# Optimization experiments

Hardware: AMD Instinct MI355X
Metric: run time of the kernel (lower is better)

## Reference

```python
import jax, jax.numpy as jnp
import numpy as np

N = 2048  # nodes; num_node_features == N per __init__
E = 65536 # directed edges (avg degree 32)
H1, H2 = 32, 20


def setup_inputs() -> dict:
    key = jax.random.key(0)
    ks = jax.random.split(key, 10)
    u = lambda k, shape, fan: jax.random.uniform(k, shape, jnp.float32, -1.0, 1.0) / np.sqrt(fan)
    x = jax.random.normal(ks[0], (N, N), jnp.float32)
    edge_index = jax.random.randint(ks[1], (2, E), 0, N, jnp.int64)
    return {
        'x': x,
        'edge_index': edge_index,
        'W1': u(ks[2], (N, H1), N),   'b1': u(ks[3], (H1,), N),
        'W2': u(ks[4], (H1, H2), H1), 'b2': u(ks[5], (H2,), H1),
        'aW': u(ks[6], (H2, N * N), H2), 'ab': u(ks[7], (N * N,), H2),
        'cW': u(ks[8], (H2, 1), H2),  'cb': u(ks[9], (1,), H2),
    }


def gcn_conv(x, edge_index, W, b):
    # GCNConv: D^{-1/2} (A + I) D^{-1/2} X W + b, aggregated at target nodes
    loop = jnp.arange(N)
    src = jnp.concatenate([edge_index[0], loop])
    dst = jnp.concatenate([edge_index[1], loop])
    deg = jax.ops.segment_sum(jnp.ones_like(dst, dtype=x.dtype), dst, num_segments=N)
    dinv = jnp.where(deg > 0, jax.lax.rsqrt(deg), 0.0)
    norm = dinv[src] * dinv[dst]                      # [E+N]
    h = x @ W                                         # [N, out]
    msg = h[src] * norm[:, None]                      # gather + scale
    return jax.ops.segment_sum(msg, dst, num_segments=N) + b


def reference(x, edge_index, W1, b1, W2, b2, aW, ab, cW, cb):
    h = jax.nn.relu(gcn_conv(x, edge_index, W1, b1))
    h = jax.nn.relu(gcn_conv(h, edge_index, W2, b2))
    critic_output = (h @ cW + cb).mean(axis=0)        # [1]
    x_actor = h.mean(axis=0)                          # [20]
    logits = (x_actor @ aW + ab).reshape(N, N)
    probs = jax.nn.softmax(logits, axis=1)
    flat = probs.reshape(-1)
    # Faithful replication of the sequential two-max scan: the second 'max'
    # is the running max just before the final update, i.e. the argmax of the
    # prefix strictly before the global argmax (0,0 if argmax is at flat[0]).
    idx1 = jnp.argmax(flat)
    masked = jnp.where(jnp.arange(N * N) < idx1, flat, -jnp.inf)
    idx2 = jnp.argmax(masked)  # argmax over all -inf -> 0, matching (si,sj)=(0,0)
    actions = jnp.stack([
        jnp.stack([idx1 // N, idx1 % N]),
        jnp.stack([idx2 // N, idx2 % N]),
    ])  # [2, 2] int
    # Faithful to original: indexes the FLATTENED probs with the (i,j) pairs
    log_probs = -jnp.log(flat[actions])               # [2, 2]
    return actions, log_probs, critic_output
```

## Files before the change

### kernel.cpp

```cpp
#include <hip/hip_runtime.h>
#include <hip/hip_bf16.h>
#include <math.h>

#define NN_NODES 2048
#define NE 65536
#define H1C 32
#define H2C 20
#define AW_STRIDE 4194304ull

__global__ void k_deg(const int* __restrict__ ei, int* __restrict__ deg) {
    int e = blockIdx.x * 256 + threadIdx.x;
    if (e < NE) atomicAdd(&deg[ei[NE + e]], 1);
}

__global__ void k_scan(const int* __restrict__ deg, float* __restrict__ dinv,
                       int* __restrict__ off) {
    __shared__ int s[1024];
    int t = threadIdx.x;
    int d0 = deg[2 * t], d1 = deg[2 * t + 1];
    dinv[2 * t]     = rsqrtf((float)(d0 + 1));
    dinv[2 * t + 1] = rsqrtf((float)(d1 + 1));
    s[t] = d0 + d1;
    __syncthreads();
    for (int o = 1; o < 1024; o <<= 1) {
        int add = (t >= o) ? s[t - o] : 0;
        __syncthreads();
        s[t] += add;
        __syncthreads();
    }
    int excl = (t > 0) ? s[t - 1] : 0;
    off[2 * t] = excl;
    off[2 * t + 1] = excl + d0;
    if (t == 1023) off[2048] = s[1023];
}

__global__ void k_scatter(const int* __restrict__ ei, const float* __restrict__ dinv,
                          const int* __restrict__ off, int* __restrict__ cnt,
                          int* __restrict__ csr_src, float* __restrict__ csr_norm) {
    int e = blockIdx.x * 256 + threadIdx.x;
    if (e >= NE) return;
    int s = ei[e], d = ei[NE + e];
    int pos = off[d] + atomicAdd(&cnt[d], 1);
    csr_src[pos] = s;
    csr_norm[pos] = dinv[s] * dinv[d];
}

__global__ __launch_bounds__(256) void k_gemm1(const float* __restrict__ X,
                                               const float* __restrict__ W1,
                                               float* __restrict__ h_tmp) {
    __shared__ float Xs[32][33];
    __shared__ __align__(16) float Ws[32][32];
    int t = threadIdx.x;
    int rg = blockIdx.x >> 3, kc = blockIdx.x & 7;
    int r0 = rg * 32;
    int r = t >> 3, c4 = (t & 7) * 4;
    float4 acc = {0.f, 0.f, 0.f, 0.f};
    for (int kt = 0; kt < 8; ++kt) {
        int k0 = kc * 256 + kt * 32;
#pragma unroll
        for (int i = 0; i < 4; ++i) {
            int id = t + i * 256;
            int rr = id >> 5, kk = id & 31;
            Xs[rr][kk] = X[(size_t)(r0 + rr) * 2048 + k0 + kk];
            Ws[rr][kk] = W1[(size_t)(k0 + rr) * 32 + kk];
        }
        __syncthreads();
#pragma unroll
        for (int kk = 0; kk < 32; ++kk) {
            float a = Xs[r][kk];
            float4 b = *(const float4*)&Ws[kk][c4];
            acc.x += a * b.x; acc.y += a * b.y; acc.z += a * b.z; acc.w += a * b.w;
        }
        __syncthreads();
    }
    float* dst = &h_tmp[(size_t)(r0 + r) * 32 + c4];
    atomicAdd(dst + 0, acc.x);
    atomicAdd(dst + 1, acc.y);
    atomicAdd(dst + 2, acc.z);
    atomicAdd(dst + 3, acc.w);
}

template <int C>
__global__ __launch_bounds__(256) void k_agg(const float* __restrict__ h,
                                             const float* __restrict__ csr_norm,
                                             const int* __restrict__ csr_src,
                                             const int* __restrict__ off,
                                             const float* __restrict__ dinv,
                                             const float* __restrict__ bias,
                                             float* __restrict__ out) {
    int n = blockIdx.x;
    int t = threadIdx.x;
    int c = t & 31, s = t >> 5;
    __shared__ float red[8][32];
    float acc = 0.f;
    int e0 = off[n], e1 = off[n + 1];
    if (c < C) {
        for (int e = e0 + s; e < e1; e += 8) {
            int src = csr_src[e];
            acc += h[(size_t)src * C + c] * csr_norm[e];
        }
    }
    red[s][c] = acc;
    __syncthreads();
    if (t < 32) {
        float v = red[0][t];
#pragma unroll
        for (int i = 1; i < 8; ++i) v += red[i][t];
        if (t < C) {
            float dn = dinv[n];
            v += h[(size_t)n * C + t] * dn * dn + bias[t];
            out[(size_t)n * C + t] = fmaxf(v, 0.f);
        }
    }
}

__global__ __launch_bounds__(256) void k_gemm2(const float* __restrict__ h1,
                                               const float* __restrict__ W2,
                                               float* __restrict__ h2t) {
    __shared__ float Ws[H1C * H2C];
    int t = threadIdx.x;
    for (int i = t; i < H1C * H2C; i += 256) Ws[i] = W2[i];
    __syncthreads();
    int id = blockIdx.x * 256 + t;
    int n = id / 20, c = id % 20;
    const float* hr = &h1[(size_t)n * 32];
    float acc = 0.f;
#pragma unroll
    for (int k = 0; k < 32; ++k) acc += hr[k] * Ws[k * 20 + c];
    h2t[(size_t)n * 20 + c] = acc;
}

__global__ __launch_bounds__(640) void k_xa(const float* __restrict__ h2,
                                            float* __restrict__ xa_sum) {
    __shared__ float red[640];
    int t = threadIdx.x;
    int nl = t / 20, c = t % 20;
    int n = blockIdx.x * 32 + nl;
    red[t] = h2[(size_t)n * 20 + c];
    __syncthreads();
    for (int o = 16; o >= 1; o >>= 1) {
        if (nl < o) red[t] += red[(nl + o) * 20 + c];
        __syncthreads();
    }
    if (t < 20) atomicAdd(&xa_sum[t], red[t]);
}

__global__ __launch_bounds__(256) void k_rows(const float* __restrict__ aW,
                                              const float* __restrict__ ab,
                                              const float* __restrict__ xa_sum,
                                              float* __restrict__ rowM,
                                              float* __restrict__ rowZ,
                                              int* __restrict__ rowC) {
    __shared__ float xa[20];
    __shared__ float redf[256];
    __shared__ int redi[256];
    int t = threadIdx.x;
    int row = blockIdx.x;
    if (t < 20) xa[t] = xa_sum[t] * (1.0f / 2048.0f);
    __syncthreads();
    size_t base = (size_t)row * 2048;
    float l[8];
#pragma unroll
    for (int u = 0; u < 2; ++u) {
        int j0 = u * 1024 + t * 4;
        float4 acc = *(const float4*)&ab[base + j0];
#pragma unroll
        for (int k = 0; k < 20; ++k) {
            float4 w = *(const float4*)&aW[(size_t)k * AW_STRIDE + base + j0];
            float sv = xa[k];
            acc.x += sv * w.x; acc.y += sv * w.y; acc.z += sv * w.z; acc.w += sv * w.w;
        }
        l[u * 4 + 0] = acc.x; l[u * 4 + 1] = acc.y;
        l[u * 4 + 2] = acc.z; l[u * 4 + 3] = acc.w;
    }
    float m = l[0];
    int mi = t * 4;
#pragma unroll
    for (int q = 1; q < 8; ++q) {
        int col = (q >> 2) * 1024 + t * 4 + (q & 3);
        if (l[q] > m) { m = l[q]; mi = col; }
    }
    redf[t] = m; redi[t] = mi;
    __syncthreads();
    for (int o = 128; o >= 1; o >>= 1) {
        if (t < o) {
            float vo = redf[t + o]; int io = redi[t + o];
            if (vo > redf[t] || (vo == redf[t] && io < redi[t])) { redf[t] = vo; redi[t] = io; }
        }
        __syncthreads();
    }
    float M = redf[0];
    int C1 = redi[0];
    __syncthreads();
    float zsum = 0.f;
#pragma unroll
    for (int q = 0; q < 8; ++q) zsum += expf(l[q] - M);
    redf[t] = zsum;
    __syncthreads();
    for (int o = 128; o >= 1; o >>= 1) {
        if (t < o) redf[t] += redf[t + o];
        __syncthreads();
    }
    if (t == 0) { rowM[row] = M; rowZ[row] = redf[0]; rowC[row] = C1; }
}

__global__ __launch_bounds__(256) void k_final(const float* __restrict__ rowM,
                                               const float* __restrict__ rowZ,
                                               const int* __restrict__ rowC,
                                               const float* __restrict__ aW,
                                               const float* __restrict__ ab,
                                               const float* __restrict__ xa_sum,
                                               const float* __restrict__ cW,
                                               const float* __restrict__ cb,
                                               float* __restrict__ out) {
    __shared__ float xa[20];
    __shared__ float rf[256];
    __shared__ int ri[256];
    __shared__ float sM1, sZ1;
    __shared__ int sR1, sC1, sR2, sC2;
    int t = threadIdx.x;
    if (t < 20) xa[t] = xa_sum[t] * (1.0f / 2048.0f);
    __syncthreads();

    float z = INFINITY; int zi = 0x7fffffff;
    for (int i = t; i < 2048; i += 256) {
        float v = rowZ[i];
        if (v < z || (v == z && i < zi)) { z = v; zi = i; }
    }
    rf[t] = z; ri[t] = zi;
    __syncthreads();
    for (int o = 128; o >= 1; o >>= 1) {
        if (t < o) {
            float vo = rf[t + o]; int io = ri[t + o];
            if (vo < rf[t] || (vo == rf[t] && io < ri[t])) { rf[t] = vo; ri[t] = io; }
        }
        __syncthreads();
    }
    if (t == 0) {
        sR1 = ri[0]; sC1 = rowC[ri[0]]; sM1 = rowM[ri[0]]; sZ1 = rowZ[ri[0]];
    }
    __syncthreads();
    int r1 = sR1, c1 = sC1;

    z = INFINITY; zi = 0x7fffffff;
    for (int i = t; i < r1; i += 256) {
        float v = rowZ[i];
        if (v < z || (v == z && i < zi)) { z = v; zi = i; }
    }
    __syncthreads();
    rf[t] = z; ri[t] = zi;
    __syncthreads();
    for (int o = 128; o >= 1; o >>= 1) {
        if (t < o) {
            float vo = rf[t + o]; int io = ri[t + o];
            if (vo < rf[t] || (vo == rf[t] && io < ri[t])) { rf[t] = vo; ri[t] = io; }
        }
        __syncthreads();
    }
    float ZP = rf[0]; int iP = ri[0];
    __syncthreads();

    float lm = -INFINITY; int lj = 0x7fffffff;
    size_t base = (size_t)r1 * 2048;
    for (int j = t; j < c1; j += 256) {
        float acc = ab[base + j];
#pragma unroll
        for (int k = 0; k < 20; ++k) acc += xa[k] * aW[(size_t)k * AW_STRIDE + base + j];
        if (acc > lm) { lm = acc; lj = j; }
    }
    rf[t] = lm; ri[t] = lj;
    __syncthreads();
    for (int o = 128; o >= 1; o >>= 1) {
        if (t < o) {
            float vo = rf[t + o]; int io = ri[t + o];
            if (vo > rf[t] || (vo == rf[t] && io < ri[t])) { rf[t] = vo; ri[t] = io; }
        }
        __syncthreads();
    }
    float LB = rf[0]; int jB = ri[0];
    __syncthreads();

    if (t == 0) {
        int r2, c2;
        if (r1 == 0 && c1 == 0) {
            r2 = 0; c2 = 0;
        } else {
            bool hasA = (r1 > 0), hasB = (c1 > 0);
            float pA = hasA ? 1.0f / ZP : -INFINITY;
            float pB = hasB ? expf(LB - sM1) / sZ1 : -INFINITY;
            if (hasB && (!hasA || pB > pA)) { r2 = r1; c2 = jB; }
            else                            { r2 = iP; c2 = rowC[iP]; }
        }
        sR2 = r2; sC2 = c2;
        out[0] = (float)r1; out[1] = (float)c1;
        out[2] = (float)r2; out[3] = (float)c2;
        float cr = 0.f;
#pragma unroll
        for (int k = 0; k < 20; ++k) cr += xa[k] * cW[k];
        out[8] = cr + cb[0];
    }
    __syncthreads();

    if (t < 4) {
        int a = (t == 0) ? sR1 : (t == 1) ? sC1 : (t == 2) ? sR2 : sC2;
        float acc = ab[a];
#pragma unroll
        for (int k = 0; k < 20; ++k) acc += xa[k] * aW[(size_t)k * AW_STRIDE + a];
        float lp = (acc - rowM[0]) - logf(rowZ[0]);
        out[4 + t] = -lp;
    }
}

extern "C" void kernel_launch(void* const* d_in, const int* in_sizes, int n_in,
                              void* d_out, int out_size, void* d_ws, size_t ws_size,
                              hipStream_t stream) {
    const float* x  = (const float*)d_in[0];
    const int*   ei = (const int*)d_in[1];
    const float* W1 = (const float*)d_in[2];
    const float* b1 = (const float*)d_in[3];
    const float* W2 = (const float*)d_in[4];
    const float* b2 = (const float*)d_in[5];
    const float* aW = (const float*)d_in[6];
    const float* ab = (const float*)d_in[7];
    const float* cW = (const float*)d_in[8];
    const float* cb = (const float*)d_in[9];
    float* out = (float*)d_out;

    char* p = (char*)d_ws;
    auto alloc = [&](size_t bytes) {
        void* r = (void*)p;
        p += (bytes + 255) & ~(size_t)255;
        return r;
    };
    int*   deg    = (int*)alloc(2048 * 4);
    int*   cnt    = (int*)alloc(2048 * 4);
    float* xa_sum = (float*)alloc(64 * 4);
    float* h_tmp  = (float*)alloc(65536 * 4);
    size_t zero_bytes = (size_t)(p - (char*)d_ws);
    float* dinv     = (float*)alloc(2048 * 4);
    int*   csr_off  = (int*)alloc(2049 * 4);
    int*   csr_src  = (int*)alloc(65536 * 4);
    float* csr_norm = (float*)alloc(65536 * 4);
    float* h1       = (float*)alloc(65536 * 4);
    float* h2t      = (float*)alloc(40960 * 4);
    float* h2       = (float*)alloc(40960 * 4);
    float* rowM     = (float*)alloc(2048 * 4);
    float* rowZ     = (float*)alloc(2048 * 4);
    int*   rowC     = (int*)alloc(2048 * 4);

    hipMemsetAsync(d_ws, 0, zero_bytes, stream);
    k_deg<<<NE / 256, 256, 0, stream>>>(ei, deg);
    k_scan<<<1, 1024, 0, stream>>>(deg, dinv, csr_off);
    k_scatter<<<NE / 256, 256, 0, stream>>>(ei, dinv, csr_off, cnt, csr_src, csr_norm);
    k_gemm1<<<512, 256, 0, stream>>>(x, W1, h_tmp);
    k_agg<32><<<2048, 256, 0, stream>>>(h_tmp, csr_norm, csr_src, csr_off, dinv, b1, h1);
    k_gemm2<<<160, 256, 0, stream>>>(h1, W2, h2t);
    k_agg<20><<<2048, 256, 0, stream>>>(h2t, csr_norm, csr_src, csr_off, dinv, b2, h2);
    k_xa<<<64, 640, 0, stream>>>(h2, xa_sum);
    k_rows<<<2048, 256, 0, stream>>>(aW, ab, xa_sum, rowM, rowZ, rowC);
    k_final<<<1, 256, 0, stream>>>(rowM, rowZ, rowC, aW, ab, xa_sum, cW, cb, out);
}
```

Measured before the change: 543.0 us.

## Fuse GCN layers with gemm2, mean-pool, and final argmax via last-block ticket

Fuses the second-layer weight multiply into the first aggregation kernel, folds the mean-pool atomic into the second aggregation, and merges the final selection into the row-softmax kernel using a last-block-done atomic counter. This removes three kernel launches and the h1/h2 intermediate buffers. In exchange, xa_sum now receives 2048×20 atomics to a single small location. The last-block pattern adds threadfence and serialises the final reduction onto one block. The remaining kernels are dominated by the aW streaming in k_rows, so the launch savings are small relative to the total.

```diff
diff --git a/kernel.cpp b/kernel.cpp
--- a/kernel.cpp
+++ b/kernel.cpp
@@ -80,77 +80,87 @@
     atomicAdd(dst + 3, acc.w);
 }
 
-template <int C>
-__global__ __launch_bounds__(256) void k_agg(const float* __restrict__ h,
-                                             const float* __restrict__ csr_norm,
-                                             const int* __restrict__ csr_src,
-                                             const int* __restrict__ off,
-                                             const float* __restrict__ dinv,
-                                             const float* __restrict__ bias,
-                                             float* __restrict__ out) {
+__global__ __launch_bounds__(256) void k_agg1(const float* __restrict__ h_tmp,
+                                              const float* __restrict__ csr_norm,
+                                              const int* __restrict__ csr_src,
+                                              const int* __restrict__ off,
+                                              const float* __restrict__ dinv,
+                                              const float* __restrict__ b1,
+                                              const float* __restrict__ W2,
+                                              float* __restrict__ h2t) {
+    int n = blockIdx.x;
+    int t = threadIdx.x;
+    int c = t & 31, s = t >> 5;
+    __shared__ float red[8][32];
+    __shared__ float W2s[H1C * H2C];
+    __shared__ float h1row[H1C];
+    for (int i = t; i < H1C * H2C; i += 256) W2s[i] = W2[i];
+    float acc = 0.f;
+    int e0 = off[n], e1 = off[n + 1];
+    for (int e = e0 + s; e < e1; e += 8) {
+        int src = csr_src[e];
+        acc += h_tmp[(size_t)src * H1C + c] * csr_norm[e];
+    }
+    red[s][c] = acc;
+    __syncthreads();
+    if (t < 32) {
+        float v = red[0][t];
+#pragma unroll
+        for (int i = 1; i < 8; ++i) v += red[i][t];
+        float dn = dinv[n];
+        v += h_tmp[(size_t)n * H1C + t] * dn * dn + b1[t];
+        h1row[t] = fmaxf(v, 0.f);
+    }
+    __syncthreads();
+    if (t < H2C) {
+        float a2 = 0.f;
+#pragma unroll
+        for (int k = 0; k < H1C; ++k) a2 += h1row[k] * W2s[k * H2C + t];
+        h2t[(size_t)n * H2C + t] = a2;
+    }
+}
+
+__global__ __launch_bounds__(256) void k_agg2(const float* __restrict__ h2t,
+                                              const float* __restrict__ csr_norm,
+                                              const int* __restrict__ csr_src,
+                                              const int* __restrict__ off,
+                                              const float* __restrict__ dinv,
+                                              const float* __restrict__ b2,
+                                              float* __restrict__ xa_sum) {
     int n = blockIdx.x;
     int t = threadIdx.x;
     int c = t & 31, s = t >> 5;
     __shared__ float red[8][32];
     float acc = 0.f;
     int e0 = off[n], e1 = off[n + 1];
-    if (c < C) {
+    if (c < H2C) {
         for (int e = e0 + s; e < e1; e += 8) {
             int src = csr_src[e];
-            acc += h[(size_t)src * C + c] * csr_norm[e];
+            acc += h2t[(size_t)src * H2C + c] * csr_norm[e];
         }
     }
     red[s][c] = acc;
     __syncthreads();
-    if (t < 32) {
+    if (t < H2C) {
         float v = red[0][t];
 #pragma unroll
         for (int i = 1; i < 8; ++i) v += red[i][t];
-        if (t < C) {
-            float dn = dinv[n];
-            v += h[(size_t)n * C + t] * dn * dn + bias[t];
-            out[(size_t)n * C + t] = fmaxf(v, 0.f);
-        }
-    }
-}
-
-__global__ __launch_bounds__(256) void k_gemm2(const float* __restrict__ h1,
-                                               const float* __restrict__ W2,
-                                               float* __restrict__ h2t) {
-    __shared__ float Ws[H1C * H2C];
-    int t = threadIdx.x;
-    for (int i = t; i < H1C * H2C; i += 256) Ws[i] = W2[i];
-    __syncthreads();
-    int id = blockIdx.x * 256 + t;
-    int n = id / 20, c = id % 20;
-    const float* hr = &h1[(size_t)n * 32];
-    float acc = 0.f;
-#pragma unroll
-    for (int k = 0; k < 32; ++k) acc += hr[k] * Ws[k * 20 + c];
-    h2t[(size_t)n * 20 + c] = acc;
-}
-
-__global__ __launch_bounds__(640) void k_xa(const float* __restrict__ h2,
-                                            float* __restrict__ xa_sum) {
-    __shared__ float red[640];
-    int t = threadIdx.x;
-    int nl = t / 20, c = t % 20;
-    int n = blockIdx.x * 32 + nl;
-    red[t] = h2[(size_t)n * 20 + c];
-    __syncthreads();
-    for (int o = 16; o >= 1; o >>= 1) {
-        if (nl < o) red[t] += red[(nl + o) * 20 + c];
-        __syncthreads();
-    }
-    if (t < 20) atomicAdd(&xa_sum[t], red[t]);
-}
-
-__global__ __launch_bounds__(256) void k_rows(const float* __restrict__ aW,
-                                              const float* __restrict__ ab,
-                                              const float* __restrict__ xa_sum,
-                                              float* __restrict__ rowM,
-                                              float* __restrict__ rowZ,
-                                              int* __restrict__ rowC) {
+        float dn = dinv[n];
+        v += h2t[(size_t)n * H2C + t] * dn * dn + b2[t];
+        atomicAdd(&xa_sum[t], fmaxf(v, 0.f));
+    }
+}
+
+__global__ __launch_bounds__(256) void k_rows_final(const float* __restrict__ aW,
+                                                    const float* __restrict__ ab,
+                                                    const float* __restrict__ xa_sum,
+                                                    float* __restrict__ rowM,
+                                                    float* __restrict__ rowZ,
+                                                    int* __restrict__ rowC,
+                                                    unsigned int* __restrict__ counter,
+                                                    const float* __restrict__ cW,
+                                                    const float* __restrict__ cb,
+                                                    float* __restrict__ out) {
     __shared__ float xa[20];
     __shared__ float redf[256];
     __shared__ int redi[256];
@@ -202,25 +212,18 @@
         __syncthreads();
     }
     if (t == 0) { rowM[row] = M; rowZ[row] = redf[0]; rowC[row] = C1; }
-}
-
-__global__ __launch_bounds__(256) void k_final(const float* __restrict__ rowM,
-                                               const float* __restrict__ rowZ,
-                                               const int* __restrict__ rowC,
-                                               const float* __restrict__ aW,
-                                               const float* __restrict__ ab,
-                                               const float* __restrict__ xa_sum,
-                                               const float* __restrict__ cW,
-                                               const float* __restrict__ cb,
-                                               float* __restrict__ out) {
-    __shared__ float xa[20];
+
+    __threadfence();
+    __shared__ unsigned int sTicket;
+    if (t == 0) sTicket = atomicAdd(counter, 1u);
+    __syncthreads();
+    if (sTicket != 2047u) return;
+    __threadfence();
+
     __shared__ float rf[256];
     __shared__ int ri[256];
     __shared__ float sM1, sZ1;
     __shared__ int sR1, sC1, sR2, sC2;
-    int t = threadIdx.x;
-    if (t < 20) xa[t] = xa_sum[t] * (1.0f / 2048.0f);
-    __syncthreads();
 
     float z = INFINITY; int zi = 0x7fffffff;
     for (int i = t; i < 2048; i += 256) {
@@ -261,11 +264,11 @@
     __syncthreads();
 
     float lm = -INFINITY; int lj = 0x7fffffff;
-    size_t base = (size_t)r1 * 2048;
+    size_t base1 = (size_t)r1 * 2048;
     for (int j = t; j < c1; j += 256) {
-        float acc = ab[base + j];
-#pragma unroll
-        for (int k = 0; k < 20; ++k) acc += xa[k] * aW[(size_t)k * AW_STRIDE + base + j];
+        float acc = ab[base1 + j];
+#pragma unroll
+        for (int k = 0; k < 20; ++k) acc += xa[k] * aW[(size_t)k * AW_STRIDE + base1 + j];
         if (acc > lm) { lm = acc; lj = j; }
     }
     rf[t] = lm; ri[t] = lj;
@@ -332,18 +335,17 @@
         p += (bytes + 255) & ~(size_t)255;
         return r;
     };
-    int*   deg    = (int*)alloc(2048 * 4);
-    int*   cnt    = (int*)alloc(2048 * 4);
-    float* xa_sum = (float*)alloc(64 * 4);
-    float* h_tmp  = (float*)alloc(65536 * 4);
+    int*          deg     = (int*)alloc(2048 * 4);
+    int*          cnt     = (int*)alloc(2048 * 4);
+    float*        xa_sum  = (float*)alloc(64 * 4);
+    unsigned int* counter = (unsigned int*)alloc(64 * 4);
+    float*        h_tmp   = (float*)alloc(65536 * 4);
     size_t zero_bytes = (size_t)(p - (char*)d_ws);
     float* dinv     = (float*)alloc(2048 * 4);
     int*   csr_off  = (int*)alloc(2049 * 4);
     int*   csr_src  = (int*)alloc(65536 * 4);
     float* csr_norm = (float*)alloc(65536 * 4);
-    float* h1       = (float*)alloc(65536 * 4);
     float* h2t      = (float*)alloc(40960 * 4);
-    float* h2       = (float*)alloc(40960 * 4);
     float* rowM     = (float*)alloc(2048 * 4);
     float* rowZ     = (float*)alloc(2048 * 4);
     int*   rowC     = (int*)alloc(2048 * 4);
@@ -353,10 +355,7 @@
     k_scan<<<1, 1024, 0, stream>>>(deg, dinv, csr_off);
     k_scatter<<<NE / 256, 256, 0, stream>>>(ei, dinv, csr_off, cnt, csr_src, csr_norm);
     k_gemm1<<<512, 256, 0, stream>>>(x, W1, h_tmp);
-    k_agg<32><<<2048, 256, 0, stream>>>(h_tmp, csr_norm, csr_src, csr_off, dinv, b1, h1);
-    k_gemm2<<<160, 256, 0, stream>>>(h1, W2, h2t);
-    k_agg<20><<<2048, 256, 0, stream>>>(h2t, csr_norm, csr_src, csr_off, dinv, b2, h2);
-    k_xa<<<64, 640, 0, stream>>>(h2, xa_sum);
-    k_rows<<<2048, 256, 0, stream>>>(aW, ab, xa_sum, rowM, rowZ, rowC);
-    k_final<<<1, 256, 0, stream>>>(rowM, rowZ, rowC, aW, ab, xa_sum, cW, cb, out);
-}
+    k_agg1<<<2048, 256, 0, stream>>>(h_tmp, csr_norm, csr_src, csr_off, dinv, b1, W2, h2t);
+    k_agg2<<<2048, 256, 0, stream>>>(h2t, csr_norm, csr_src, csr_off, dinv, b2, xa_sum);
+    k_rows_final<<<2048, 256, 0, stream>>>(aW, ab, xa_sum, rowM, rowZ, rowC, counter, cW, cb, out);
+}
```

Measured after the change: 992.3 us. 1.83x slower.
